# Performance work log

Measured on AMD Instinct MI355X. Metric: run time of the kernel, lower is better.

The kernel has to match this reference:

```python
import jax, jax.numpy as jnp
import numpy as np

NUM_EXPERTS = 8
MAX_ENTROPY = float(np.log(NUM_EXPERTS))
# fixed (non-learnable) fusion weights, matching register_buffer defaults
W_ENTROPY, W_CONF, W_MISMATCH, W_SEMANTIC, W_EIGEN = 0.25, -0.2, 0.2, 0.2, 0.15

B, S, H, D = 1024, 512, 512, 2048


def setup_inputs() -> dict:
    key = jax.random.key(0)
    ks = jax.random.split(key, 8)
    return {
        "routing_entropy": jax.random.uniform(ks[0], (B,), dtype=jnp.float32),
        "moe_confidence": jax.random.uniform(ks[1], (B,), dtype=jnp.float32),
        "memory_mismatch": jax.random.normal(ks[2], (B,), dtype=jnp.float32),
        "memory_loss": jax.random.uniform(ks[3], (B,), dtype=jnp.float32),
        "hidden_states": jax.random.normal(ks[4], (B, S, H), dtype=jnp.float32),
        "routing_repr": jax.random.normal(ks[5], (B, D), dtype=jnp.float32),
        "probe_w": jax.random.normal(ks[6], (H,), dtype=jnp.float32) * (1.0 / np.sqrt(H)),
        "probe_b": jnp.zeros((1,), dtype=jnp.float32),
    }


def reference(routing_entropy, moe_confidence, memory_mismatch, memory_loss,
              hidden_states, routing_repr, probe_w, probe_b):
    # normalized routing entropy
    norm_entropy = routing_entropy / MAX_ENTROPY                      # (B,)
    inv_confidence = 1.0 - moe_confidence                             # (B,)
    norm_mismatch = jax.nn.sigmoid(memory_mismatch - 2.0)             # (B,)

    # SemanticEntropyProbe: per-token linear->sigmoid, mean over sequence
    logits = jnp.einsum('bsh,h->bs', hidden_states, probe_w) + probe_b[0]
    semantic_entropy = jax.nn.sigmoid(logits).mean(axis=1)            # (B,)

    # EigenScore: SVD of a single (1, D) row has exactly one singular value,
    # equal to the row's L2 norm -> vectorized norm replaces per-sample SVD loop.
    sv = jnp.linalg.norm(routing_repr, axis=-1)                       # (B,)
    eigen_score = 1.0 / (sv + 1e-8)                                   # (B,)
    norm_eigen = jax.nn.sigmoid(eigen_score - 1.0)                    # (B,)

    risk = (W_ENTROPY * norm_entropy + W_CONF * inv_confidence
            + W_MISMATCH * norm_mismatch + W_SEMANTIC * semantic_entropy
            + W_EIGEN * norm_eigen)
    risk_clamped = jnp.clip(risk, 0.0, 1.0)                           # (B,)
    return risk_clamped
```

## Files before the change

### kernel.cpp

```cpp
#include <hip/hip_runtime.h>
#include <hip/hip_bf16.h>
#include <math.h>


#define S_TOK 512
#define H_DIM 512
#define D_DIM 2048

__device__ __forceinline__ float sigmoidf_fast(float x) {
    return 1.0f / (1.0f + __expf(-x));
}

__global__ __launch_bounds__(256) void halluc_kernel(
    const float* __restrict__ routing_entropy,
    const float* __restrict__ moe_confidence,
    const float* __restrict__ memory_mismatch,
    const float* __restrict__ hidden_states,
    const float* __restrict__ routing_repr,
    const float* __restrict__ probe_w,
    const float* __restrict__ probe_b,
    float* __restrict__ out)
{
    const int b    = blockIdx.x;
    const int tid  = threadIdx.x;
    const int lane = tid & 63;
    const int wave = tid >> 6;

    const float4* pw4 = (const float4*)probe_w;
    const float4 w0 = pw4[lane];
    const float4 w1 = pw4[lane + 64];
    const float  pb = probe_b[0];

    const float4* hs4 = (const float4*)(hidden_states + (size_t)b * S_TOK * H_DIM);
    float sem = 0.0f;
    #pragma unroll 2
    for (int s = wave; s < S_TOK; s += 4) {
        const float4* row = hs4 + (size_t)s * (H_DIM / 4);
        const float4 a0 = row[lane];
        const float4 a1 = row[lane + 64];
        float d = a0.x * w0.x + a0.y * w0.y + a0.z * w0.z + a0.w * w0.w
                + a1.x * w1.x + a1.y * w1.y + a1.z * w1.z + a1.w * w1.w;
        #pragma unroll
        for (int m = 32; m > 0; m >>= 1) d += __shfl_xor(d, m, 64);
        sem += sigmoidf_fast(d + pb);
    }

    const float4* rr4 = (const float4*)(routing_repr + (size_t)b * D_DIM);
    const float4 r0 = rr4[tid];
    const float4 r1 = rr4[tid + 256];
    float sq = r0.x * r0.x + r0.y * r0.y + r0.z * r0.z + r0.w * r0.w
             + r1.x * r1.x + r1.y * r1.y + r1.z * r1.z + r1.w * r1.w;
    #pragma unroll
    for (int m = 32; m > 0; m >>= 1) sq += __shfl_xor(sq, m, 64);

    __shared__ float s_sem[4];
    __shared__ float s_sq[4];
    if (lane == 0) { s_sem[wave] = sem; s_sq[wave] = sq; }
    __syncthreads();

    if (tid == 0) {
        const float sem_mean = (s_sem[0] + s_sem[1] + s_sem[2] + s_sem[3]) * (1.0f / S_TOK);
        const float sv       = sqrtf(s_sq[0] + s_sq[1] + s_sq[2] + s_sq[3]);
        const float neig     = sigmoidf_fast(1.0f / (sv + 1e-8f) - 1.0f);

        const float ne = routing_entropy[b] * 0.48089834696298783f;
        const float ic = 1.0f - moe_confidence[b];
        const float nm = sigmoidf_fast(memory_mismatch[b] - 2.0f);

        float risk = 0.25f * ne - 0.2f * ic + 0.2f * nm
                   + 0.2f * sem_mean + 0.15f * neig;
        risk = fminf(fmaxf(risk, 0.0f), 1.0f);
        out[b] = risk;
    }
}

extern "C" void kernel_launch(void* const* d_in, const int* in_sizes, int n_in,
                              void* d_out, int out_size, void* d_ws, size_t ws_size,
                              hipStream_t stream) {
    const float* routing_entropy = (const float*)d_in[0];
    const float* moe_confidence  = (const float*)d_in[1];
    const float* memory_mismatch = (const float*)d_in[2];
    const float* hidden_states   = (const float*)d_in[4];
    const float* routing_repr    = (const float*)d_in[5];
    const float* probe_w         = (const float*)d_in[6];
    const float* probe_b         = (const float*)d_in[7];
    float* out = (float*)d_out;

    const int B = in_sizes[0];

    halluc_kernel<<<B, 256, 0, stream>>>(
        routing_entropy, moe_confidence, memory_mismatch,
        hidden_states, routing_repr, probe_w, probe_b, out);
}
```

Baseline: 1.330 ms.

## Process four tokens per wave with register double-buffered row prefetch

Each wave now splits into four 16-lane groups, each handling its own token row. The next row is loaded into registers while the current one is reduced, so more loads are in flight and the shuffle reduction is shorter (four steps instead of six). The sum over the groups is combined at the end. Launch bounds now request four blocks per CU, which limits registers while the kernel holds more live float4 buffers.

Result: no change. 1.323 ms (-0.6%).

```diff
diff --git a/kernel.cpp b/kernel.cpp
--- a/kernel.cpp
+++ b/kernel.cpp
@@ -1,17 +1,20 @@
 #include <hip/hip_runtime.h>
-#include <hip/hip_bf16.h>
 #include <math.h>
 
 
 #define S_TOK 512
 #define H_DIM 512
 #define D_DIM 2048
+#define H4    128
 
 __device__ __forceinline__ float sigmoidf_fast(float x) {
     return 1.0f / (1.0f + __expf(-x));
 }
+__device__ __forceinline__ float dot4(float4 a, float4 b) {
+    return a.x * b.x + a.y * b.y + a.z * b.z + a.w * b.w;
+}
 
-__global__ __launch_bounds__(256) void halluc_kernel(
+__global__ __launch_bounds__(256, 4) void halluc_kernel(
     const float* __restrict__ routing_entropy,
     const float* __restrict__ moe_confidence,
     const float* __restrict__ memory_mismatch,
@@ -25,25 +28,59 @@
     const int tid  = threadIdx.x;
     const int lane = tid & 63;
     const int wave = tid >> 6;
+    const int u    = lane & 15;
 
     const float4* pw4 = (const float4*)probe_w;
-    const float4 w0 = pw4[lane];
-    const float4 w1 = pw4[lane + 64];
-    const float  pb = probe_b[0];
+    float4 w[8];
+    #pragma unroll
+    for (int c = 0; c < 8; ++c) w[c] = pw4[u + 16 * c];
+    const float pb = probe_b[0];
 
     const float4* hs4 = (const float4*)(hidden_states + (size_t)b * S_TOK * H_DIM);
+    const int t0 = wave * 4 + (lane >> 4);
+
+    float4 bufA[4], bufB[4];
+    {
+        const float4* row = hs4 + (size_t)t0 * H4;
+        #pragma unroll
+        for (int c = 0; c < 4; ++c) bufA[c] = row[u + 16 * c];
+        #pragma unroll
+        for (int c = 0; c < 4; ++c) bufB[c] = row[u + 16 * c + 64];
+    }
+
     float sem = 0.0f;
+
+    auto consume = [&](const float4* A, const float4* Bv) {
+        float d0 = dot4(A[0],  w[0]) + dot4(A[2],  w[2]);
+        float d1 = dot4(A[1],  w[1]) + dot4(A[3],  w[3]);
+        float d2 = dot4(Bv[0], w[4]) + dot4(Bv[2], w[6]);
+        float d3 = dot4(Bv[1], w[5]) + dot4(Bv[3], w[7]);
+        float d  = (d0 + d1) + (d2 + d3);
+        d += __shfl_xor(d, 8, 64);
+        d += __shfl_xor(d, 4, 64);
+        d += __shfl_xor(d, 2, 64);
+        d += __shfl_xor(d, 1, 64);
+        sem += sigmoidf_fast(d + pb);
+    };
+
     #pragma unroll 2
-    for (int s = wave; s < S_TOK; s += 4) {
-        const float4* row = hs4 + (size_t)s * (H_DIM / 4);
-        const float4 a0 = row[lane];
-        const float4 a1 = row[lane + 64];
-        float d = a0.x * w0.x + a0.y * w0.y + a0.z * w0.z + a0.w * w0.w
-                + a1.x * w1.x + a1.y * w1.y + a1.z * w1.z + a1.w * w1.w;
+    for (int it = 0; it < 31; ++it) {
+        const float4* nrow = hs4 + (size_t)(t0 + 16 * (it + 1)) * H4;
+        float4 nA[4], nB[4];
         #pragma unroll
-        for (int m = 32; m > 0; m >>= 1) d += __shfl_xor(d, m, 64);
-        sem += sigmoidf_fast(d + pb);
+        for (int c = 0; c < 4; ++c) nA[c] = nrow[u + 16 * c];
+        #pragma unroll
+        for (int c = 0; c < 4; ++c) nB[c] = nrow[u + 16 * c + 64];
+
+        consume(bufA, bufB);
+
+        #pragma unroll
+        for (int c = 0; c < 4; ++c) { bufA[c] = nA[c]; bufB[c] = nB[c]; }
     }
+    consume(bufA, bufB);
+
+    sem += __shfl_xor(sem, 16, 64);
+    sem += __shfl_xor(sem, 32, 64);
 
     const float4* rr4 = (const float4*)(routing_repr + (size_t)b * D_DIM);
     const float4 r0 = rr4[tid];
```

## Split into grid-stride token sigmoid pass and per-batch fuse pass

Applied to the files above, without the earlier changes.

Splits the single per-batch kernel into two launches. The first is a grid-stride kernel over all tokens: it computes each token's probe dot product and sigmoid, handles two tokens per iteration to keep more loads in flight, and writes the results to workspace. The second kernel reduces those per-token values per batch and computes the fused risk score. The aim is to decouple parallelism from the batch count and raise memory-level parallelism, at the cost of an extra launch and a small intermediate write and read.

Result: no change. 1.343 ms (+1.0%).

```diff
diff --git a/kernel.cpp b/kernel.cpp
--- a/kernel.cpp
+++ b/kernel.cpp
@@ -1,24 +1,72 @@
 #include <hip/hip_runtime.h>
-#include <hip/hip_bf16.h>
 #include <math.h>
 
 
 #define S_TOK 512
 #define H_DIM 512
 #define D_DIM 2048
+#define H4    (H_DIM / 4)
 
 __device__ __forceinline__ float sigmoidf_fast(float x) {
     return 1.0f / (1.0f + __expf(-x));
 }
+__device__ __forceinline__ float dot4(float4 a, float4 b) {
+    return a.x * b.x + a.y * b.y + a.z * b.z + a.w * b.w;
+}
 
-__global__ __launch_bounds__(256) void halluc_kernel(
+__global__ __launch_bounds__(256, 4) void sem_pass(
+    const float* __restrict__ hidden_states,
+    const float* __restrict__ probe_w,
+    const float* __restrict__ probe_b,
+    float* __restrict__ tok_sig,
+    int total_tokens)
+{
+    const int lane = threadIdx.x & 63;
+    const int wave = threadIdx.x >> 6;
+    const int gw   = blockIdx.x * 4 + wave;
+    const int nw   = gridDim.x * 4;
+
+    const float4* pw4 = (const float4*)probe_w;
+    const float4 w0 = pw4[lane];
+    const float4 w1 = pw4[lane + 64];
+    const float  pb = probe_b[0];
+
+    const float4* hs4 = (const float4*)hidden_states;
+
+    for (int t = gw; t < total_tokens; t += 2 * nw) {
+        const float4* r0 = hs4 + (size_t)t * H4;
+        const float4 a0 = r0[lane];
+        const float4 a1 = r0[lane + 64];
+
+        const int t2 = t + nw;
+        float4 b0 = make_float4(0.f, 0.f, 0.f, 0.f);
+        float4 b1 = make_float4(0.f, 0.f, 0.f, 0.f);
+        if (t2 < total_tokens) {
+            const float4* r1 = hs4 + (size_t)t2 * H4;
+            b0 = r1[lane];
+            b1 = r1[lane + 64];
+        }
+
+        float d = dot4(a0, w0) + dot4(a1, w1);
+        float e = dot4(b0, w0) + dot4(b1, w1);
+        #pragma unroll
+        for (int m = 32; m > 0; m >>= 1) {
+            d += __shfl_xor(d, m, 64);
+            e += __shfl_xor(e, m, 64);
+        }
+        if (lane == 0) {
+            tok_sig[t] = sigmoidf_fast(d + pb);
+            if (t2 < total_tokens) tok_sig[t2] = sigmoidf_fast(e + pb);
+        }
+    }
+}
+
+__global__ __launch_bounds__(256) void fuse_pass(
     const float* __restrict__ routing_entropy,
     const float* __restrict__ moe_confidence,
     const float* __restrict__ memory_mismatch,
-    const float* __restrict__ hidden_states,
     const float* __restrict__ routing_repr,
-    const float* __restrict__ probe_w,
-    const float* __restrict__ probe_b,
+    const float* __restrict__ tok_sig,
     float* __restrict__ out)
 {
     const int b    = blockIdx.x;
@@ -26,32 +74,19 @@
     const int lane = tid & 63;
     const int wave = tid >> 6;
 
-    const float4* pw4 = (const float4*)probe_w;
-    const float4 w0 = pw4[lane];
-    const float4 w1 = pw4[lane + 64];
-    const float  pb = probe_b[0];
-
-    const float4* hs4 = (const float4*)(hidden_states + (size_t)b * S_TOK * H_DIM);
-    float sem = 0.0f;
-    #pragma unroll 2
-    for (int s = wave; s < S_TOK; s += 4) {
-        const float4* row = hs4 + (size_t)s * (H_DIM / 4);
-        const float4 a0 = row[lane];
-        const float4 a1 = row[lane + 64];
-        float d = a0.x * w0.x + a0.y * w0.y + a0.z * w0.z + a0.w * w0.w
-                + a1.x * w1.x + a1.y * w1.y + a1.z * w1.z + a1.w * w1.w;
-        #pragma unroll
-        for (int m = 32; m > 0; m >>= 1) d += __shfl_xor(d, m, 64);
-        sem += sigmoidf_fast(d + pb);
-    }
+    const float* ts = tok_sig + (size_t)b * S_TOK;
+    float sem = ts[tid] + ts[tid + 256];
 
     const float4* rr4 = (const float4*)(routing_repr + (size_t)b * D_DIM);
     const float4 r0 = rr4[tid];
     const float4 r1 = rr4[tid + 256];
-    float sq = r0.x * r0.x + r0.y * r0.y + r0.z * r0.z + r0.w * r0.w
-             + r1.x * r1.x + r1.y * r1.y + r1.z * r1.z + r1.w * r1.w;
+    float sq = dot4(r0, r0) + dot4(r1, r1);
+
     #pragma unroll
-    for (int m = 32; m > 0; m >>= 1) sq += __shfl_xor(sq, m, 64);
+    for (int m = 32; m > 0; m >>= 1) {
+        sem += __shfl_xor(sem, m, 64);
+        sq  += __shfl_xor(sq,  m, 64);
+    }
 
     __shared__ float s_sem[4];
     __shared__ float s_sq[4];
@@ -87,8 +122,13 @@
     float* out = (float*)d_out;
 
     const int B = in_sizes[0];
+    const int total_tokens = B * S_TOK;
 
-    halluc_kernel<<<B, 256, 0, stream>>>(
-        routing_entropy, moe_confidence, memory_mismatch,
-        hidden_states, routing_repr, probe_w, probe_b, out);
+    float* tok_sig = (float*)d_ws;
+
+    sem_pass<<<4096, 256, 0, stream>>>(hidden_states, probe_w, probe_b,
+                                       tok_sig, total_tokens);
+    fuse_pass<<<B, 256, 0, stream>>>(routing_entropy, moe_confidence,
+                                     memory_mismatch, routing_repr,
+                                     tok_sig, out);
 }
```
